# Performance work log

Hardware: AMD Instinct MI355X
Metric: run time of the kernel (lower is better)

The kernel has to match this reference:

```python
import jax, jax.numpy as jnp
import numpy as np

N = 50000        # drug nodes
R = 64           # relations (side effects)
E = 20000        # edges per relation
B = 16           # bases
IN = 256
OUT = 256


def setup_inputs() -> dict:
    key = jax.random.key(0)
    ks = jax.random.split(key, 7)
    x = jax.random.normal(ks[0], (N, IN), dtype=jnp.float32)
    att = jax.random.normal(ks[1], (R, B), dtype=jnp.float32) / np.sqrt(B)
    basis = jax.random.normal(ks[2], (B, IN, OUT), dtype=jnp.float32) / np.sqrt(IN)
    root = jax.random.normal(ks[3], (IN, OUT), dtype=jnp.float32) / np.sqrt(IN)
    # per-destination-node degree normalizer (strictly positive, like edge counts)
    dest_deg = jax.random.uniform(ks[4], (N, 1), dtype=jnp.float32) * 9.0 + 1.0
    edge_src = jax.random.randint(ks[5], (R, E), 0, N, dtype=jnp.int64)
    edge_dst = jax.random.randint(ks[6], (R, E), 0, N, dtype=jnp.int64)
    return {"x": x, "att": att, "basis": basis, "root": root,
            "dest_deg": dest_deg, "edge_src": edge_src, "edge_dst": edge_dst}


def reference(x, att, basis, root, dest_deg, edge_src, edge_dst):
    # basis decomposition: w[r] = sum_b att[r,b] * basis[b]
    w = jnp.einsum('rb,bio->rio', att, basis)          # [R, IN, OUT]
    # per-relation gather + transform: messages along each edge
    x_src = x[edge_src]                                 # [R, E, IN]
    msgs = jnp.einsum('rei,rio->reo', x_src, w)         # [R, E, OUT]
    # scatter-sum to destinations, summed over all relations (HeteroConv aggr='sum')
    agg = jax.ops.segment_sum(msgs.reshape(-1, OUT),
                              edge_dst.reshape(-1),
                              num_segments=N)           # [N, OUT]
    out = agg / dest_deg + x @ root                     # [N, OUT]
    return out
```

## Files before the change

kernel.cpp:

```cpp
#include <hip/hip_runtime.h>
#include <stdint.h>

#define NN 50000
#define RR 64
#define EE 20000
#define NB 16
#define IND 256
#define OUTD 256
#define KK 4352
#define NE (RR * EE)
#define GITER 68
#define SCANB 49

typedef __attribute__((ext_vector_type(8))) short bf16x8;
typedef __attribute__((ext_vector_type(4))) float f32x4;
typedef __attribute__((ext_vector_type(2))) float f32x2;

__device__ __forceinline__ unsigned short f2bf(float f) {
  union { float f; unsigned u; } v; v.f = f;
  unsigned r = v.u + 0x7FFFu + ((v.u >> 16) & 1u);
  return (unsigned short)(r >> 16);
}
__device__ __forceinline__ float asf(unsigned u) {
  union { unsigned u; float f; } v; v.u = u; return v.f;
}

__global__ __launch_bounds__(256) void k_xbf(const float* __restrict__ x,
                                             unsigned short* __restrict__ xb) {
  const int gt = blockIdx.x * 256 + threadIdx.x;
  const size_t g = (size_t)gt * 8;
  const int row = gt >> 5;
  const int k = (gt & 31) * 8;
  float4 v0 = *reinterpret_cast<const float4*>(x + g);
  float4 v1 = *reinterpret_cast<const float4*>(x + g + 4);
  union { bf16x8 v; unsigned short u[8]; } pk;
  pk.u[0]=f2bf(v0.x); pk.u[1]=f2bf(v0.y); pk.u[2]=f2bf(v0.z); pk.u[3]=f2bf(v0.w);
  pk.u[4]=f2bf(v1.x); pk.u[5]=f2bf(v1.y); pk.u[6]=f2bf(v1.z); pk.u[7]=f2bf(v1.w);
  const int tile = k >> 6, ch = (k >> 3) & 7;
  *reinterpret_cast<bf16x8*>(
      xb + (size_t)row * 256 + tile * 64 + ((ch ^ (row & 7)) << 3)) = pk.v;
}

__global__ __launch_bounds__(256) void k_hist(const int* __restrict__ edst,
                                              int* __restrict__ cnt) {
  const int g = blockIdx.x * 256 + threadIdx.x;
  atomicAdd(&cnt[edst[g]], 1);
}

__global__ __launch_bounds__(256) void k_scan_a(const int* __restrict__ cnt,
                                                int* __restrict__ rowptr,
                                                int* __restrict__ bsum) {
  __shared__ int ps[256];
  const int t = threadIdx.x, blk = blockIdx.x;
  const int base = blk * 1024 + t * 4;
  int v[4];
#pragma unroll
  for (int q = 0; q < 4; ++q) {
    const int idx = base + q;
    v[q] = (idx < NN) ? cnt[idx] : 0;
  }
  const int s = v[0] + v[1] + v[2] + v[3];
  ps[t] = s;
  __syncthreads();
  for (int off = 1; off < 256; off <<= 1) {
    const int u = (t >= off) ? ps[t - off] : 0;
    __syncthreads();
    ps[t] += u;
    __syncthreads();
  }
  int run = ps[t] - s;
#pragma unroll
  for (int q = 0; q < 4; ++q) {
    const int idx = base + q;
    if (idx < NN) rowptr[idx] = run;
    run += v[q];
  }
  if (t == 255) bsum[blk] = ps[255];
}

__global__ __launch_bounds__(64) void k_scan_b(const int* __restrict__ bsum,
                                               int* __restrict__ boff,
                                               int* __restrict__ rowptr) {
  const int t = threadIdx.x;
  const int own = (t < SCANB) ? bsum[t] : 0;
  int v = own;
  for (int off = 1; off < 64; off <<= 1) {
    const int u = __shfl_up(v, off);
    if (t >= off) v += u;
  }
  if (t < SCANB) boff[t] = v - own;
  if (t == SCANB - 1) rowptr[NN] = v;
}

__global__ __launch_bounds__(256) void k_scan_c(const int* __restrict__ boff,
                                                int* __restrict__ rowptr,
                                                int* __restrict__ wof) {
  const int t = threadIdx.x, blk = blockIdx.x;
  const int base = blk * 1024 + t * 4;
  const int bo = boff[blk];
#pragma unroll
  for (int q = 0; q < 4; ++q) {
    const int idx = base + q;
    if (idx < NN) {
      const int val = rowptr[idx] + bo;
      rowptr[idx] = val;
      wof[idx] = val;
    }
  }
}

__global__ __launch_bounds__(256) void k_scatter(const int* __restrict__ esrc,
                                                 const int* __restrict__ edst,
                                                 int* __restrict__ wof,
                                                 unsigned* __restrict__ payload) {
  const int g = blockIdx.x * 256 + threadIdx.x;
  const int d = edst[g];
  const int src = esrc[g];
  const int r = g / EE;
  const int pos = atomicAdd(&wof[d], 1);
  payload[pos] = ((unsigned)r << 18) | (unsigned)src;
}

__global__ __launch_bounds__(256) void k_bt(const float* __restrict__ basis,
                                            const float* __restrict__ root,
                                            unsigned short* __restrict__ bt) {
  const int o = blockIdx.x;
  for (int k = threadIdx.x; k < KK; k += 256) {
    float v;
    if (k < 4096) v = basis[(size_t)k * 256 + o];
    else          v = root[(size_t)(k - 4096) * 256 + o];
    const int tile = k >> 6, ch = (k >> 3) & 7;
    bt[(size_t)o * KK + tile * 64 + ((ch ^ (o & 7)) << 3) + (k & 7)] = f2bf(v);
  }
}

__global__ __launch_bounds__(256) void k_vbuild(
    const unsigned short* __restrict__ xbf, const float* __restrict__ att,
    const float* __restrict__ deg, const int* __restrict__ rowptr,
    const unsigned* __restrict__ payload, unsigned short* __restrict__ Vb,
    const int c0) {
  __shared__ float attl[RR * NB];
  const int t = threadIdx.x;
  *reinterpret_cast<float4*>(&attl[t * 4]) =
      *reinterpret_cast<const float4*>(&att[t * 4]);
  __syncthreads();
  const int lane = t & 63;
  const int n = c0 + blockIdx.x * 4 + (t >> 6);
  if (n >= NN) return;
  const int k0 = rowptr[n], k1 = rowptr[n + 1];

  const int laneBase = (lane >> 4) * 64 + (lane & 1) * 4;
  const unsigned laneCh = (unsigned)((lane >> 1) & 7);

  f32x2 acc2[NB][2];
#pragma unroll
  for (int b = 0; b < NB; ++b) {
    acc2[b][0] = (f32x2){0.f, 0.f};
    acc2[b][1] = (f32x2){0.f, 0.f};
  }

#define XLOAD(PK)                                                            \
  (*reinterpret_cast<const uint2*>(                                          \
      xbf + (size_t)((PK) & 0x3FFFFu) * 256 + laneBase +                     \
      ((laneCh ^ (((PK) & 7u))) << 3)))

  unsigned pkA = 0, pkB = 0;
  uint2 xvA = {0, 0}, xvB = {0, 0};
  if (k0 < k1)     { pkA = payload[k0];     xvA = XLOAD(pkA); }
  if (k0 + 1 < k1) { pkB = payload[k0 + 1]; xvB = XLOAD(pkB); }
  for (int k = k0; k < k1; ++k) {
    unsigned pkC = 0; uint2 xvC = {0, 0};
    if (k + 2 < k1) { pkC = payload[k + 2]; xvC = XLOAD(pkC); }
    const int r = (int)(pkA >> 18);
    const f32x2 x01 = {asf(xvA.x << 16), asf(xvA.x & 0xFFFF0000u)};
    const f32x2 x23 = {asf(xvA.y << 16), asf(xvA.y & 0xFFFF0000u)};
#pragma unroll
    for (int b4 = 0; b4 < 4; ++b4) {
      const float4 a4 = *reinterpret_cast<const float4*>(&attl[r * NB + b4 * 4]);
      const float aa[4] = {a4.x, a4.y, a4.z, a4.w};
#pragma unroll
      for (int q = 0; q < 4; ++q) {
        const int b = b4 * 4 + q;
        acc2[b][0] += aa[q] * x01;
        acc2[b][1] += aa[q] * x23;
      }
    }
    pkA = pkB; xvA = xvB; pkB = pkC; xvB = xvC;
  }
  const float iv = 1.0f / deg[n];
  const int nl = n - c0;
  unsigned short* vr = Vb + (size_t)nl * 4096 + (lane >> 4) * 64 +
                       ((laneCh ^ (unsigned)(nl & 7)) << 3) + (lane & 1) * 4;
#pragma unroll
  for (int b = 0; b < NB; ++b) {
    ushort4 s;
    s.x = f2bf(acc2[b][0].x * iv); s.y = f2bf(acc2[b][0].y * iv);
    s.z = f2bf(acc2[b][1].x * iv); s.w = f2bf(acc2[b][1].y * iv);
    *reinterpret_cast<ushort4*>(vr + (size_t)b * 256) = s;
  }
}

__global__ __launch_bounds__(256) void k_gemm4(
    const unsigned short* __restrict__ Vb, const unsigned short* __restrict__ xbf,
    const unsigned short* __restrict__ bt, float* __restrict__ out, const int c0) {
  __shared__ unsigned short As[2][128 * 64];
  __shared__ unsigned short Bs[2][128 * 64];
  const int t = threadIdx.x;
  const int rb = blockIdx.x, cb = blockIdx.y;
  const int lane = t & 63, w = t >> 6;
  const int wr = w >> 1, wc = w & 1;
  const int lc = lane & 15, lg = lane >> 4;

  const int lrow8 = lane >> 3;
  const int lchk  = lane & 7;
  const int arow0 = rb * 128 + w * 32 + lrow8;
  const int bcol0 = cb * 128 + w * 32 + lrow8;
  const unsigned short* vrow = Vb  + (size_t)arow0 * 4096 + lchk * 8;
  const unsigned short* xrow = xbf + (size_t)(c0 + arow0) * 256 + lchk * 8;
  const unsigned short* brow = bt  + (size_t)bcol0 * KK + lchk * 8;

#define GL(G, L) __builtin_amdgcn_global_load_lds(                            \
    (const __attribute__((address_space(1))) unsigned int*)(G),               \
    (__attribute__((address_space(3))) unsigned int*)(L), 16, 0, 0)

#define STAGE4(IT, BUF)                                                       \
  {                                                                           \
    const int it_ = (IT);                                                     \
    unsigned short* abase = &As[BUF][w * 2048];                               \
    unsigned short* bbase = &Bs[BUF][w * 2048];                               \
    if (it_ < 64) {                                                           \
      const unsigned short* ga = vrow + it_ * 64;                             \
      _Pragma("unroll")                                                       \
      for (int i = 0; i < 4; ++i) GL(ga + (size_t)i * 8 * 4096, abase + i * 512); \
    } else {                                                                  \
      const unsigned short* ga = xrow + (it_ - 64) * 64;                      \
      _Pragma("unroll")                                                       \
      for (int i = 0; i < 4; ++i) GL(ga + (size_t)i * 8 * 256, abase + i * 512); \
    }                                                                         \
    const unsigned short* gb = brow + it_ * 64;                               \
    _Pragma("unroll")                                                         \
    for (int i = 0; i < 4; ++i) GL(gb + (size_t)i * 8 * KK, bbase + i * 512); \
  }

  f32x4 acc[4][4];
  const f32x4 zf = {0.f, 0.f, 0.f, 0.f};
#pragma unroll
  for (int m = 0; m < 4; ++m)
#pragma unroll
    for (int n = 0; n < 4; ++n) acc[m][n] = zf;

  STAGE4(0, 0);
  asm volatile("s_waitcnt vmcnt(0)" ::: "memory");
  __syncthreads();
  int cur = 0;
  for (int it = 0; it < GITER; ++it) {
    if (it + 1 < GITER) STAGE4(it + 1, cur ^ 1);
#pragma unroll
    for (int kk = 0; kk < 2; ++kk) {
      bf16x8 af[4], bfm[4];
      const int ch = kk * 4 + lg;
#pragma unroll
      for (int m = 0; m < 4; ++m) {
        const int r2 = wr * 64 + m * 16 + lc;
        af[m] = *reinterpret_cast<const bf16x8*>(&As[cur][r2 * 64 + ((ch ^ (r2 & 7)) << 3)]);
      }
#pragma unroll
      for (int n = 0; n < 4; ++n) {
        const int c2 = wc * 64 + n * 16 + lc;
        bfm[n] = *reinterpret_cast<const bf16x8*>(&Bs[cur][c2 * 64 + ((ch ^ (c2 & 7)) << 3)]);
      }
#pragma unroll
      for (int m = 0; m < 4; ++m)
#pragma unroll
        for (int n = 0; n < 4; ++n)
          acc[m][n] = __builtin_amdgcn_mfma_f32_16x16x32_bf16(af[m], bfm[n], acc[m][n], 0, 0, 0);
    }
    asm volatile("s_waitcnt vmcnt(0)" ::: "memory");
    __syncthreads();
    cur ^= 1;
  }
#pragma unroll
  for (int m = 0; m < 4; ++m) {
#pragma unroll
    for (int j = 0; j < 4; ++j) {
      const int n = c0 + rb * 128 + wr * 64 + m * 16 + lg * 4 + j;
      if (n < NN) {
        float* orow = out + (size_t)n * OUTD + cb * 128 + wc * 64 + lc;
        orow[0]  = acc[m][0][j];
        orow[16] = acc[m][1][j];
        orow[32] = acc[m][2][j];
        orow[48] = acc[m][3][j];
      }
    }
  }
}

extern "C" void kernel_launch(void* const* d_in, const int* in_sizes, int n_in,
                              void* d_out, int out_size, void* d_ws, size_t ws_size,
                              hipStream_t stream) {
  (void)in_sizes; (void)n_in; (void)out_size;
  const float* x     = (const float*)d_in[0];
  const float* att   = (const float*)d_in[1];
  const float* basis = (const float*)d_in[2];
  const float* root  = (const float*)d_in[3];
  const float* deg   = (const float*)d_in[4];
  const int*   esrc  = (const int*)d_in[5];
  const int*   edst  = (const int*)d_in[6];
  float* out = (float*)d_out;

  char* p = (char*)d_ws;
  unsigned short* xbf = (unsigned short*)p; p += (size_t)NN * IND * 2;
  unsigned short* bt  = (unsigned short*)p; p += (size_t)OUTD * KK * 2;
  unsigned* payload   = (unsigned*)p;       p += (size_t)NE * 4;
  int* rowptr         = (int*)p;            p += (size_t)(NN + 1) * 4;
  int* wof            = (int*)p;            p += (size_t)NN * 4;
  int* cnt            = (int*)p;            p += (size_t)NN * 4;
  int* bsum           = (int*)p;            p += 64 * 4;
  int* boff           = (int*)p;            p += 64 * 4;
  uintptr_t up = ((uintptr_t)p + 255) & ~(uintptr_t)255;
  unsigned short* Vb  = (unsigned short*)up;
  const size_t used = (size_t)((char*)Vb - (char*)d_ws);
  const size_t avail = ws_size - used;

  int chunk;
  if      (avail >= (size_t)(NN + 128) * 4096 * 2) chunk = NN;
  else if (avail >= (size_t)25600 * 4096 * 2)      chunk = 25600;
  else                                             chunk = 12800;

  hipMemsetAsync(cnt, 0, (size_t)NN * 4, stream);
  hipLaunchKernelGGL(k_xbf,     dim3(NN * IND / 2048), dim3(256),  0, stream, x, xbf);
  hipLaunchKernelGGL(k_hist,    dim3(NE / 256),        dim3(256),  0, stream, edst, cnt);
  hipLaunchKernelGGL(k_scan_a,  dim3(SCANB),           dim3(256),  0, stream, cnt, rowptr, bsum);
  hipLaunchKernelGGL(k_scan_b,  dim3(1),               dim3(64),   0, stream, bsum, boff, rowptr);
  hipLaunchKernelGGL(k_scan_c,  dim3(SCANB),           dim3(256),  0, stream, boff, rowptr, wof);
  hipLaunchKernelGGL(k_scatter, dim3(NE / 256),        dim3(256),  0, stream, esrc, edst, wof, payload);
  hipLaunchKernelGGL(k_bt,      dim3(OUTD),            dim3(256),  0, stream, basis, root, bt);

  for (int c0 = 0; c0 < NN; c0 += chunk) {
    const int rows = (NN - c0 < chunk) ? (NN - c0) : chunk;
    hipLaunchKernelGGL(k_vbuild, dim3((rows + 3) / 4), dim3(256), 0, stream,
                       xbf, att, deg, rowptr, payload, Vb, c0);
    hipLaunchKernelGGL(k_gemm4, dim3((rows + 127) / 128, 2), dim3(256), 0, stream,
                       Vb, xbf, bt, out, c0);
  }
}
```

Before: 653.5 us.

## Split bf16 x into linear and swizzled copies, single-buffer GEMM, nontemporal stores

The conversion kernel now writes x as bf16 twice: a linear copy for the gather in vbuild and a swizzled copy for the GEMM. Each vbuild lane then reads contiguous 8-byte chunks with no per-edge XOR address math. The GEMM drops LDS double buffering for a single buffer with a load-wait-sync per K step, which halves shared memory (more blocks per CU) but gives up load/compute overlap. Vb and output stores become nontemporal to avoid polluting cache.

```diff
diff --git a/kernel.cpp b/kernel.cpp
--- a/kernel.cpp
+++ b/kernel.cpp
@@ -15,6 +15,7 @@
 typedef __attribute__((ext_vector_type(8))) short bf16x8;
 typedef __attribute__((ext_vector_type(4))) float f32x4;
 typedef __attribute__((ext_vector_type(2))) float f32x2;
+typedef __attribute__((ext_vector_type(2))) unsigned int u32x2;
 
 __device__ __forceinline__ unsigned short f2bf(float f) {
   union { float f; unsigned u; } v; v.f = f;
@@ -26,7 +27,8 @@
 }
 
 __global__ __launch_bounds__(256) void k_xbf(const float* __restrict__ x,
-                                             unsigned short* __restrict__ xb) {
+                                             unsigned short* __restrict__ xlin,
+                                             unsigned short* __restrict__ xsw) {
   const int gt = blockIdx.x * 256 + threadIdx.x;
   const size_t g = (size_t)gt * 8;
   const int row = gt >> 5;
@@ -36,9 +38,10 @@
   union { bf16x8 v; unsigned short u[8]; } pk;
   pk.u[0]=f2bf(v0.x); pk.u[1]=f2bf(v0.y); pk.u[2]=f2bf(v0.z); pk.u[3]=f2bf(v0.w);
   pk.u[4]=f2bf(v1.x); pk.u[5]=f2bf(v1.y); pk.u[6]=f2bf(v1.z); pk.u[7]=f2bf(v1.w);
+  *reinterpret_cast<bf16x8*>(xlin + g) = pk.v;
   const int tile = k >> 6, ch = (k >> 3) & 7;
   *reinterpret_cast<bf16x8*>(
-      xb + (size_t)row * 256 + tile * 64 + ((ch ^ (row & 7)) << 3)) = pk.v;
+      xsw + (size_t)row * 256 + tile * 64 + ((ch ^ (row & 7)) << 3)) = pk.v;
 }
 
 __global__ __launch_bounds__(256) void k_hist(const int* __restrict__ edst,
@@ -135,7 +138,7 @@
 }
 
 __global__ __launch_bounds__(256) void k_vbuild(
-    const unsigned short* __restrict__ xbf, const float* __restrict__ att,
+    const unsigned short* __restrict__ xlin, const float* __restrict__ att,
     const float* __restrict__ deg, const int* __restrict__ rowptr,
     const unsigned* __restrict__ payload, unsigned short* __restrict__ Vb,
     const int c0) {
@@ -149,9 +152,6 @@
   if (n >= NN) return;
   const int k0 = rowptr[n], k1 = rowptr[n + 1];
 
-  const int laneBase = (lane >> 4) * 64 + (lane & 1) * 4;
-  const unsigned laneCh = (unsigned)((lane >> 1) & 7);
-
   f32x2 acc2[NB][2];
 #pragma unroll
   for (int b = 0; b < NB; ++b) {
@@ -161,8 +161,7 @@
 
 #define XLOAD(PK)                                                            \
   (*reinterpret_cast<const uint2*>(                                          \
-      xbf + (size_t)((PK) & 0x3FFFFu) * 256 + laneBase +                     \
-      ((laneCh ^ (((PK) & 7u))) << 3)))
+      xlin + (size_t)((PK) & 0x3FFFFu) * 256 + lane * 4))
 
   unsigned pkA = 0, pkB = 0;
   uint2 xvA = {0, 0}, xvB = {0, 0};
@@ -190,21 +189,26 @@
   const float iv = 1.0f / deg[n];
   const int nl = n - c0;
   unsigned short* vr = Vb + (size_t)nl * 4096 + (lane >> 4) * 64 +
-                       ((laneCh ^ (unsigned)(nl & 7)) << 3) + (lane & 1) * 4;
+                       ((((unsigned)(lane >> 1) & 7u) ^ (unsigned)(nl & 7)) << 3) +
+                       (lane & 1) * 4;
 #pragma unroll
   for (int b = 0; b < NB; ++b) {
-    ushort4 s;
-    s.x = f2bf(acc2[b][0].x * iv); s.y = f2bf(acc2[b][0].y * iv);
-    s.z = f2bf(acc2[b][1].x * iv); s.w = f2bf(acc2[b][1].y * iv);
-    *reinterpret_cast<ushort4*>(vr + (size_t)b * 256) = s;
-  }
-}
-
-__global__ __launch_bounds__(256) void k_gemm4(
-    const unsigned short* __restrict__ Vb, const unsigned short* __restrict__ xbf,
+    const unsigned short s0 = f2bf(acc2[b][0].x * iv);
+    const unsigned short s1 = f2bf(acc2[b][0].y * iv);
+    const unsigned short s2 = f2bf(acc2[b][1].x * iv);
+    const unsigned short s3 = f2bf(acc2[b][1].y * iv);
+    u32x2 pk;
+    pk.x = (unsigned)s0 | ((unsigned)s1 << 16);
+    pk.y = (unsigned)s2 | ((unsigned)s3 << 16);
+    __builtin_nontemporal_store(pk, reinterpret_cast<u32x2*>(vr + (size_t)b * 256));
+  }
+}
+
+__global__ __launch_bounds__(256) void k_gemm5(
+    const unsigned short* __restrict__ Vb, const unsigned short* __restrict__ xsw,
     const unsigned short* __restrict__ bt, float* __restrict__ out, const int c0) {
-  __shared__ unsigned short As[2][128 * 64];
-  __shared__ unsigned short Bs[2][128 * 64];
+  __shared__ unsigned short As[128 * 64];
+  __shared__ unsigned short Bs[128 * 64];
   const int t = threadIdx.x;
   const int rb = blockIdx.x, cb = blockIdx.y;
   const int lane = t & 63, w = t >> 6;
@@ -216,18 +220,18 @@
   const int arow0 = rb * 128 + w * 32 + lrow8;
   const int bcol0 = cb * 128 + w * 32 + lrow8;
   const unsigned short* vrow = Vb  + (size_t)arow0 * 4096 + lchk * 8;
-  const unsigned short* xrow = xbf + (size_t)(c0 + arow0) * 256 + lchk * 8;
+  const unsigned short* xrow = xsw + (size_t)(c0 + arow0) * 256 + lchk * 8;
   const unsigned short* brow = bt  + (size_t)bcol0 * KK + lchk * 8;
 
 #define GL(G, L) __builtin_amdgcn_global_load_lds(                            \
     (const __attribute__((address_space(1))) unsigned int*)(G),               \
     (__attribute__((address_space(3))) unsigned int*)(L), 16, 0, 0)
 
-#define STAGE4(IT, BUF)                                                       \
+#define STAGE4(IT)                                                            \
   {                                                                           \
     const int it_ = (IT);                                                     \
-    unsigned short* abase = &As[BUF][w * 2048];                               \
-    unsigned short* bbase = &Bs[BUF][w * 2048];                               \
+    unsigned short* abase = &As[w * 2048];                                    \
+    unsigned short* bbase = &Bs[w * 2048];                                    \
     if (it_ < 64) {                                                           \
       const unsigned short* ga = vrow + it_ * 64;                             \
       _Pragma("unroll")                                                       \
@@ -249,12 +253,11 @@
 #pragma unroll
     for (int n = 0; n < 4; ++n) acc[m][n] = zf;
 
-  STAGE4(0, 0);
-  asm volatile("s_waitcnt vmcnt(0)" ::: "memory");
-  __syncthreads();
-  int cur = 0;
   for (int it = 0; it < GITER; ++it) {
-    if (it + 1 < GITER) STAGE4(it + 1, cur ^ 1);
+    __syncthreads();
+    STAGE4(it);
+    asm volatile("s_waitcnt vmcnt(0)" ::: "memory");
+    __syncthreads();
 #pragma unroll
     for (int kk = 0; kk < 2; ++kk) {
       bf16x8 af[4], bfm[4];
@@ -262,12 +265,12 @@
 #pragma unroll
       for (int m = 0; m < 4; ++m) {
         const int r2 = wr * 64 + m * 16 + lc;
-        af[m] = *reinterpret_cast<const bf16x8*>(&As[cur][r2 * 64 + ((ch ^ (r2 & 7)) << 3)]);
+        af[m] = *reinterpret_cast<const bf16x8*>(&As[r2 * 64 + ((ch ^ (r2 & 7)) << 3)]);
       }
 #pragma unroll
       for (int n = 0; n < 4; ++n) {
         const int c2 = wc * 64 + n * 16 + lc;
-        bfm[n] = *reinterpret_cast<const bf16x8*>(&Bs[cur][c2 * 64 + ((ch ^ (c2 & 7)) << 3)]);
+        bfm[n] = *reinterpret_cast<const bf16x8*>(&Bs[c2 * 64 + ((ch ^ (c2 & 7)) << 3)]);
       }
 #pragma unroll
       for (int m = 0; m < 4; ++m)
@@ -275,9 +278,6 @@
         for (int n = 0; n < 4; ++n)
           acc[m][n] = __builtin_amdgcn_mfma_f32_16x16x32_bf16(af[m], bfm[n], acc[m][n], 0, 0, 0);
     }
-    asm volatile("s_waitcnt vmcnt(0)" ::: "memory");
-    __syncthreads();
-    cur ^= 1;
   }
 #pragma unroll
   for (int m = 0; m < 4; ++m) {
@@ -286,10 +286,10 @@
       const int n = c0 + rb * 128 + wr * 64 + m * 16 + lg * 4 + j;
       if (n < NN) {
         float* orow = out + (size_t)n * OUTD + cb * 128 + wc * 64 + lc;
-        orow[0]  = acc[m][0][j];
-        orow[16] = acc[m][1][j];
-        orow[32] = acc[m][2][j];
-        orow[48] = acc[m][3][j];
+        __builtin_nontemporal_store(acc[m][0][j], orow + 0);
+        __builtin_nontemporal_store(acc[m][1][j], orow + 16);
+        __builtin_nontemporal_store(acc[m][2][j], orow + 32);
+        __builtin_nontemporal_store(acc[m][3][j], orow + 48);
       }
     }
   }
@@ -309,14 +309,15 @@
   float* out = (float*)d_out;
 
   char* p = (char*)d_ws;
-  unsigned short* xbf = (unsigned short*)p; p += (size_t)NN * IND * 2;
-  unsigned short* bt  = (unsigned short*)p; p += (size_t)OUTD * KK * 2;
-  unsigned* payload   = (unsigned*)p;       p += (size_t)NE * 4;
-  int* rowptr         = (int*)p;            p += (size_t)(NN + 1) * 4;
-  int* wof            = (int*)p;            p += (size_t)NN * 4;
-  int* cnt            = (int*)p;            p += (size_t)NN * 4;
-  int* bsum           = (int*)p;            p += 64 * 4;
-  int* boff           = (int*)p;            p += 64 * 4;
+  unsigned short* xlin = (unsigned short*)p; p += (size_t)NN * IND * 2;
+  unsigned short* xsw  = (unsigned short*)p; p += (size_t)NN * IND * 2;
+  unsigned short* bt   = (unsigned short*)p; p += (size_t)OUTD * KK * 2;
+  unsigned* payload    = (unsigned*)p;       p += (size_t)NE * 4;
+  int* rowptr          = (int*)p;            p += (size_t)(NN + 1) * 4;
+  int* wof             = (int*)p;            p += (size_t)NN * 4;
+  int* cnt             = (int*)p;            p += (size_t)NN * 4;
+  int* bsum            = (int*)p;            p += 64 * 4;
+  int* boff            = (int*)p;            p += 64 * 4;
   uintptr_t up = ((uintptr_t)p + 255) & ~(uintptr_t)255;
   unsigned short* Vb  = (unsigned short*)up;
   const size_t used = (size_t)((char*)Vb - (char*)d_ws);
@@ -328,7 +329,7 @@
   else                                             chunk = 12800;
 
   hipMemsetAsync(cnt, 0, (size_t)NN * 4, stream);
-  hipLaunchKernelGGL(k_xbf,     dim3(NN * IND / 2048), dim3(256),  0, stream, x, xbf);
+  hipLaunchKernelGGL(k_xbf,     dim3(NN * IND / 2048), dim3(256),  0, stream, x, xlin, xsw);
   hipLaunchKernelGGL(k_hist,    dim3(NE / 256),        dim3(256),  0, stream, edst, cnt);
   hipLaunchKernelGGL(k_scan_a,  dim3(SCANB),           dim3(256),  0, stream, cnt, rowptr, bsum);
   hipLaunchKernelGGL(k_scan_b,  dim3(1),               dim3(64),   0, stream, bsum, boff, rowptr);
@@ -339,8 +340,8 @@
   for (int c0 = 0; c0 < NN; c0 += chunk) {
     const int rows = (NN - c0 < chunk) ? (NN - c0) : chunk;
     hipLaunchKernelGGL(k_vbuild, dim3((rows + 3) / 4), dim3(256), 0, stream,
-                       xbf, att, deg, rowptr, payload, Vb, c0);
-    hipLaunchKernelGGL(k_gemm4, dim3((rows + 127) / 128, 2), dim3(256), 0, stream,
-                       Vb, xbf, bt, out, c0);
-  }
-}
+                       xlin, att, deg, rowptr, payload, Vb, c0);
+    hipLaunchKernelGGL(k_gemm5, dim3((rows + 127) / 128, 2), dim3(256), 0, stream,
+                       Vb, xsw, bt, out, c0);
+  }
+}
```

Result: slower. 892.5 us (+36.6%).
